# Kernel tuning notes

Measured on AMD Instinct MI355X. Metric: run time of the kernel, lower is better.

Reference implementation:

```python
import jax, jax.numpy as jnp
import numpy as np

IMG = 640.0
CONF_THRE = 0.05
NMS_THRE = 0.5
MAX_DET = 100          # fixed NMS output slots (padded with zeros / valid-masked)
PRE_NMS_TOPK = 1000    # candidates kept before NMS
NEG = -1e9
CLS_OFFSET = 4096.0    # batched_nms class-offset trick (> max coordinate)


def _make_anchors():
    # YOLO-style grid anchors: 3 scales per location, strides 8/16/32 -> N = 25200
    levels = []
    for s in (8, 16, 32):
        g = int(IMG) // s
        c = (np.arange(g, dtype=np.float32) + 0.5) * s
        cy, cx = np.meshgrid(c, c, indexing="ij")
        cx, cy = cx.reshape(-1), cy.reshape(-1)
        for scale in (0.5, 1.0, 2.0):
            w = s * 4.0 * scale
            levels.append(np.stack([cx - w / 2, cy - w / 2, cx + w / 2, cy + w / 2], 1))
    return np.concatenate(levels, 0).astype(np.float32)  # [25200, 4]


def setup_inputs() -> dict:
    key = jax.random.key(0)
    k1, k2 = jax.random.split(key)
    B, N, C = 16, 25200, 80
    return {
        "proposals_regs": jax.random.uniform(k1, (B, N, 5), dtype=jnp.float32),
        "proposals_clses": jax.random.uniform(k2, (B, N, C), dtype=jnp.float32),
        "anchors": jnp.asarray(_make_anchors()),
    }


def _decode(deltas, anchors):
    # standard delta decode relative to anchors, then clip to image (clip_bboxes)
    aw = anchors[:, 2] - anchors[:, 0]
    ah = anchors[:, 3] - anchors[:, 1]
    acx = (anchors[:, 0] + anchors[:, 2]) * 0.5
    acy = (anchors[:, 1] + anchors[:, 3]) * 0.5
    cx = acx + deltas[:, 0] * aw
    cy = acy + deltas[:, 1] * ah
    w = aw * jnp.exp(deltas[:, 2])
    h = ah * jnp.exp(deltas[:, 3])
    boxes = jnp.stack([cx - w / 2, cy - h / 2, cx + w / 2, cy + h / 2], 1)
    return jnp.clip(boxes, 0.0, IMG)


def _iou_one(box, boxes):
    lt = jnp.maximum(box[:2], boxes[:, :2])
    rb = jnp.minimum(box[2:], boxes[:, 2:])
    wh = jnp.clip(rb - lt, 0.0)
    inter = wh[:, 0] * wh[:, 1]
    a = (box[2] - box[0]) * (box[3] - box[1])
    b = (boxes[:, 2] - boxes[:, 0]) * (boxes[:, 3] - boxes[:, 1])
    union = a + b - inter
    return jnp.where(union > 0, inter / union, 0.0)


def _nms(boxes, scores):
    # greedy hard NMS with fixed MAX_DET iterations (jit-safe, fixed shapes)
    def body(i, st):
        sc, keep, ks = st
        best = jnp.argmax(sc)
        keep = keep.at[i].set(best.astype(jnp.int32))
        ks = ks.at[i].set(sc[best])
        sc = jnp.where(_iou_one(boxes[best], boxes) > NMS_THRE, NEG, sc)
        sc = sc.at[best].set(NEG)
        return sc, keep, ks
    keep0 = jnp.zeros((MAX_DET,), jnp.int32)
    ks0 = jnp.full((MAX_DET,), NEG, scores.dtype)
    _, keep, ks = jax.lax.fori_loop(0, MAX_DET, body, (scores, keep0, ks0))
    return keep, ks


def _per_image(reg, cls, anchors):
    p_obj = reg[:, 4]
    boxes = _decode(reg[:, :4], anchors)                     # [N,4] clipped xyxy
    class_conf = jnp.max(cls, axis=1)
    class_pred = jax.lax.stop_gradient(jnp.argmax(cls, axis=1))
    scores = p_obj * class_conf                              # batched_nms score
    scores = jnp.where(scores >= CONF_THRE, scores, NEG)     # confidence mask
    top_s, top_i = jax.lax.top_k(scores, PRE_NMS_TOPK)
    b = boxes[top_i]
    cp = class_pred[top_i].astype(boxes.dtype)
    obj = p_obj[top_i]
    cc = class_conf[top_i]
    off_boxes = b + cp[:, None] * CLS_OFFSET                 # per-class NMS
    keep, kept_scores = _nms(off_boxes, top_s)
    valid = kept_scores > NEG * 0.5
    det = jnp.concatenate(
        [b[keep], obj[keep][:, None], cc[keep][:, None], cp[keep][:, None]], 1
    )  # [MAX_DET, 7] = x1,y1,x2,y2,obj,conf,cls (same layout as torch code)
    return jnp.where(valid[:, None], det, 0.0)


def reference(proposals_regs, proposals_clses, anchors):
    return jax.vmap(lambda r, c: _per_image(r, c, anchors))(
        proposals_regs, proposals_clses
    )  # [B, MAX_DET, 7]
```

## Files before the change

### kernel.cpp

```cpp
#include <hip/hip_runtime.h>
#include <math.h>

#define BB 16
#define NN 25200
#define NCLS 80
#define TOPK 1000
#define MAXDET 100
#define CAND_CAP 2048
#define RANKS 1024
#define HBINS 1024
#define HBASE 0xBD00u
#define BPI_C 99
static constexpr float NEGV = -1000000000.0f;
static constexpr float IMGSZ = 640.0f;

struct Meta {
  unsigned b1;
  unsigned n_true;
  unsigned cnt;
  unsigned pad;
};

__device__ __forceinline__ unsigned flipKey(float f) {
  unsigned u = __float_as_uint(f);
  return (u & 0x80000000u) ? ~u : (u | 0x80000000u);
}
__device__ __forceinline__ float unflipKey(unsigned k) {
  unsigned u = (k & 0x80000000u) ? (k & 0x7FFFFFFFu) : ~k;
  return __uint_as_float(u);
}

#define UMAX_DPP(VAR, CTRL)                                                                   \
  {                                                                                           \
    unsigned _o = (unsigned)__builtin_amdgcn_update_dpp(0, (int)(VAR), CTRL, 0xF, 0xF, true); \
    if (_o > (VAR)) (VAR) = _o;                                                               \
  }

__global__ void __launch_bounds__(256) k_zero(unsigned* __restrict__ p) {
  p[blockIdx.x * 256 + threadIdx.x] = 0u;
}

__global__ void __launch_bounds__(256) k_score(const float* __restrict__ regs,
                                               const float* __restrict__ clses,
                                               unsigned* __restrict__ keys,
                                               float* __restrict__ ccs,
                                               int* __restrict__ preds,
                                               unsigned* __restrict__ hist1) {
  int t = blockIdx.x * 256 + threadIdx.x;
  int row = t >> 1, e = t & 1;
  const float4* r4 = reinterpret_cast<const float4*>(clses + (size_t)row * NCLS);
  float best = -1.0f;
  int bi = 0;
#pragma unroll
  for (int j = 0; j < 10; ++j) {
    int f = e + 2 * j;
    float4 v = r4[f];
    int b0 = f * 4;
    if (v.x > best) { best = v.x; bi = b0 + 0; }
    if (v.y > best) { best = v.y; bi = b0 + 1; }
    if (v.z > best) { best = v.z; bi = b0 + 2; }
    if (v.w > best) { best = v.w; bi = b0 + 3; }
  }
  unsigned vb = __float_as_uint(best);
  unsigned m = vb;
  UMAX_DPP(m, 0xB1);
  unsigned t2 = (vb == m) ? (unsigned)(79 - bi) : 0u;
  UMAX_DPP(t2, 0xB1);
  if (e == 0) {
    float bestv = __uint_as_float(m);
    int bidx = 79 - (int)t2;
    float pobj = regs[(size_t)row * 5 + 4];
    float sc = pobj * bestv;
    bool pass = (sc >= 0.05f);
    float s = pass ? sc : NEGV;
    unsigned key = flipKey(s);
    keys[row] = key;
    ccs[row] = bestv;
    preds[row] = bidx;
    if (pass) {
      unsigned bin = (key >> 16) - HBASE;
      atomicAdd(&hist1[(size_t)(row / NN) * HBINS + bin], 1u);
    }
  }
}

__global__ void __launch_bounds__(256) k_scan(const unsigned* __restrict__ hist,
                                              Meta* __restrict__ meta) {
  __shared__ unsigned part[256];
  __shared__ unsigned sfx[256];
  __shared__ int s_sel;
  __shared__ unsigned s_cum;
  int img = blockIdx.x;
  int t = threadIdx.x;
  const unsigned* h = hist + (size_t)img * HBINS;
  uint4 mine = reinterpret_cast<const uint4*>(h)[t];
  unsigned s = mine.x + mine.y + mine.z + mine.w;
  if (t == 0) { s_sel = -1; s_cum = 0; }
  part[t] = s;
  sfx[t] = s;
  __syncthreads();
  for (int d = 1; d < 256; d <<= 1) {
    unsigned v = (t + d < 256) ? sfx[t + d] : 0u;
    __syncthreads();
    sfx[t] += v;
    __syncthreads();
  }
  {
    unsigned incl = sfx[t];
    unsigned excl = incl - part[t];
    if (incl >= (unsigned)TOPK && excl < (unsigned)TOPK) { s_sel = t; s_cum = excl; }
  }
  __syncthreads();
  unsigned total = sfx[0];
  if (total < (unsigned)TOPK) {
    if (t == 0) {
      meta[img].b1 = HBASE + 1;
      meta[img].n_true = total;
    }
  } else if (t == s_sel) {
    unsigned cum = s_cum;
    unsigned vals[4] = {mine.x, mine.y, mine.z, mine.w};
    int sel = 0;
    unsigned c_ge = 0;
    for (int j = 3; j >= 0; --j) {
      if (cum + vals[j] >= (unsigned)TOPK) { sel = j; c_ge = cum + vals[j]; break; }
      cum += vals[j];
    }
    meta[img].b1 = HBASE + (unsigned)(4 * t + sel);
    meta[img].n_true = (c_ge > (unsigned)TOPK) ? (unsigned)TOPK : c_ge;
  }
}

__global__ void k_compact(const float* __restrict__ regs, const float* __restrict__ anchors,
                          const unsigned* __restrict__ keys, const float* __restrict__ ccs,
                          const int* __restrict__ preds, Meta* __restrict__ meta,
                          float* __restrict__ cand) {
  const size_t S2 = (size_t)BB * CAND_CAP;
  int img = blockIdx.x / BPI_C;
  int i = (blockIdx.x % BPI_C) * 256 + threadIdx.x;
  if (i >= NN) return;
  int lane = threadIdx.x & 63;
  unsigned long long lt = (1ull << lane) - 1ull;
  size_t g = (size_t)img * NN + (size_t)i;
  unsigned key = keys[g];
  bool take = (key >> 16) >= meta[img].b1;
  unsigned long long mA = __ballot(take);
  if (!take) return;
  int leader = __builtin_ctzll(mA);
  unsigned base = 0;
  if (lane == leader) base = atomicAdd(&meta[img].cnt, (unsigned)__popcll(mA));
  base = __shfl(base, leader);
  unsigned pos = base + (unsigned)__popcll(mA & lt);
  if (pos >= CAND_CAP) return;
  const float* r = regs + g * 5;
  float d0 = r[0], d1 = r[1], d2 = r[2], d3 = r[3], obj = r[4];
  const float* a = anchors + (size_t)i * 4;
  float ax1 = a[0], ay1 = a[1], ax2 = a[2], ay2 = a[3];
  float aw = ax2 - ax1, ah = ay2 - ay1;
  float acx = (ax1 + ax2) * 0.5f, acy = (ay1 + ay2) * 0.5f;
  float cx = acx + d0 * aw, cy = acy + d1 * ah;
  float w = aw * expf(d2), h = ah * expf(d3);
  float hw = 0.5f * w, hh = 0.5f * h;
  float x1 = fminf(fmaxf(cx - hw, 0.0f), IMGSZ);
  float y1 = fminf(fmaxf(cy - hh, 0.0f), IMGSZ);
  float x2 = fminf(fmaxf(cx + hw, 0.0f), IMGSZ);
  float y2 = fminf(fmaxf(cy + hh, 0.0f), IMGSZ);
  size_t o = (size_t)img * CAND_CAP + pos;
  cand[0 * S2 + o] = x1;
  cand[1 * S2 + o] = y1;
  cand[2 * S2 + o] = x2;
  cand[3 * S2 + o] = y2;
  cand[4 * S2 + o] = obj;
  cand[5 * S2 + o] = ccs[g];
  cand[6 * S2 + o] = (float)preds[g];
  cand[7 * S2 + o] = unflipKey(key);
  reinterpret_cast<unsigned*>(cand + 8 * S2)[o] = (unsigned)i;
}

__global__ void __launch_bounds__(256) k_rank(const float* __restrict__ cand,
                                              const Meta* __restrict__ meta,
                                              float* __restrict__ boxr,
                                              float4* __restrict__ payr0,
                                              float4* __restrict__ payr1) {
  const size_t S2 = (size_t)BB * CAND_CAP;
  const int NR = BB * RANKS;
  __shared__ unsigned long long kk[CAND_CAP];
  int img = blockIdx.x >> 5;
  int part = blockIdx.x & 31;
  int tid = threadIdx.x;
  unsigned nload = meta[img].cnt;
  if (nload > CAND_CAP) nload = CAND_CAP;
  for (int i = tid; i < CAND_CAP; i += 256) {
    unsigned long long kv = 0ull;
    if (i < (int)nload) {
      float sc = cand[7 * S2 + (size_t)img * CAND_CAP + i];
      unsigned ai = reinterpret_cast<const unsigned*>(cand + 8 * S2)[(size_t)img * CAND_CAP + i];
      kv = ((unsigned long long)flipKey(sc) << 16) |
           (unsigned long long)((0x7FFFu - ai) & 0xFFFFu);
    }
    kk[i] = kv;
  }
  __syncthreads();
  int slot = part * 64 + (tid >> 2);
  int qtr = tid & 3;
  unsigned long long myk = kk[slot];
  unsigned rank = 0;
  for (int q = qtr * 512; q < qtr * 512 + 512; ++q) rank += (kk[q] > myk) ? 1u : 0u;
  rank += (unsigned)__builtin_amdgcn_update_dpp(0, (int)rank, 0xB1, 0xF, 0xF, true);
  rank += (unsigned)__builtin_amdgcn_update_dpp(0, (int)rank, 0x4E, 0xF, 0xF, true);
  if (qtr == 0 && slot < (int)nload && rank < RANKS) {
    size_t o = (size_t)img * CAND_CAP + slot;
    float x1 = cand[0 * S2 + o], y1 = cand[1 * S2 + o];
    float x2 = cand[2 * S2 + o], y2 = cand[3 * S2 + o];
    float obj = cand[4 * S2 + o], cc = cand[5 * S2 + o];
    float cp = cand[6 * S2 + o], sc = cand[7 * S2 + o];
    float offv = cp * 4096.0f;
    float a1 = x1 + offv, b1v = y1 + offv, a2 = x2 + offv, b2v = y2 + offv;
    size_t ro = (size_t)img * RANKS + rank;
    boxr[0 * NR + ro] = a1;
    boxr[1 * NR + ro] = b1v;
    boxr[2 * NR + ro] = a2;
    boxr[3 * NR + ro] = b2v;
    boxr[4 * NR + ro] = (a2 - a1) * (b2v - b1v);
    payr0[ro] = make_float4(x1, y1, x2, y2);
    payr1[ro] = make_float4(obj, cc, cp, sc);
  }
}

__global__ void __launch_bounds__(256) k_matrix(const float* __restrict__ boxr,
                                                const Meta* __restrict__ meta,
                                                unsigned long long* __restrict__ mat) {
  const int NR = BB * RANKS;
  __shared__ float sx1[RANKS], sy1[RANKS], sx2[RANKS], sy2[RANKS], sar[RANKS];
  int img = blockIdx.x >> 6;
  int part = blockIdx.x & 63;
  int tid = threadIdx.x, lane = tid & 63, wid = tid >> 6;
  for (int i = tid; i < RANKS; i += 256) {
    int g = img * RANKS + i;
    sx1[i] = boxr[0 * NR + g];
    sy1[i] = boxr[1 * NR + g];
    sx2[i] = boxr[2 * NR + g];
    sy2[i] = boxr[3 * NR + g];
    sar[i] = boxr[4 * NR + g];
  }
  unsigned n = meta[img].n_true;
  __syncthreads();
#pragma unroll
  for (int rr = 0; rr < 4; ++rr) {
    int r = part * 16 + wid * 4 + rr;
    if (r >= (int)n) continue;
    float bx1 = sx1[r], by1 = sy1[r], bx2 = sx2[r], by2 = sy2[r], bA = sar[r];
    unsigned long long* rowp = mat + ((size_t)img * RANKS + r) * 16;
#pragma unroll
    for (int w2 = 0; w2 < 16; ++w2) {
      int c = w2 * 64 + lane;
      float lx = fmaxf(bx1, sx1[c]), ly = fmaxf(by1, sy1[c]);
      float rx = fminf(bx2, sx2[c]), ry = fminf(by2, sy2[c]);
      float iw = fmaxf(rx - lx, 0.f), ih = fmaxf(ry - ly, 0.f);
      float inter = iw * ih;
      float uu = bA + sar[c] - inter;
      float ss = fmaf(2.0f, inter, -uu);
      float tt = uu * 0x1p-24f;
      bool sup = (uu > 0.f && ss > tt) || (c == r);
      unsigned long long b = __ballot(sup);
      if (lane == w2) rowp[w2] = b;
    }
  }
}

__global__ void __launch_bounds__(256, 1) k_scan2(const unsigned long long* __restrict__ mat,
                                                  const Meta* __restrict__ meta,
                                                  const float4* __restrict__ payr0,
                                                  const float4* __restrict__ payr1,
                                                  float* __restrict__ out) {
  __shared__ unsigned long long smat[RANKS * 16];
  __shared__ unsigned wins[MAXDET];
  __shared__ float4 lout4[MAXDET * 7 / 4];
  int img = blockIdx.x, tid = threadIdx.x, lane = tid & 63, wid = tid >> 6;
  const uint4* gm = reinterpret_cast<const uint4*>(mat + (size_t)img * RANKS * 16);
  uint4* sm4 = reinterpret_cast<uint4*>(smat);
  for (int i = tid; i < RANKS * 16 / 2; i += 256) sm4[i] = gm[i];
  if (tid < MAXDET) wins[tid] = 0xFFFFFFFFu;
  unsigned n = meta[img].n_true;
  __syncthreads();
  if (wid == 0) {
    unsigned long long alive = 0ull;
    if (lane < 16) {
      int lo = lane * 64;
      alive = ((int)n >= lo + 64) ? ~0ull
                                  : (((int)n > lo) ? ((1ull << ((int)n - lo)) - 1ull) : 0ull);
    }
    for (int it = 0; it < MAXDET; ++it) {
      unsigned long long any = __ballot(alive != 0ull);
      if (any == 0ull) break;
      int f = __builtin_ctzll(any);
      unsigned long long w = __shfl(alive, f);
      int r = f * 64 + __builtin_ctzll(w);
      if (lane == 0) wins[it] = (unsigned)r;
      unsigned long long rowv = (lane < 16) ? smat[r * 16 + lane] : 0ull;
      alive &= ~rowv;
    }
  }
  __syncthreads();
  if (tid < MAXDET) {
    unsigned r = wins[tid];
    float* row = reinterpret_cast<float*>(lout4) + tid * 7;
    if (r == 0xFFFFFFFFu) {
      row[0] = 0.f; row[1] = 0.f; row[2] = 0.f; row[3] = 0.f;
      row[4] = 0.f; row[5] = 0.f; row[6] = 0.f;
    } else {
      float4 p0 = payr0[(size_t)img * RANKS + r];
      float4 p1 = payr1[(size_t)img * RANKS + r];
      row[0] = p0.x; row[1] = p0.y; row[2] = p0.z; row[3] = p0.w;
      row[4] = p1.x; row[5] = p1.y; row[6] = p1.z;
    }
  }
  __syncthreads();
  float4* go4 = reinterpret_cast<float4*>(out + (size_t)img * MAXDET * 7);
  if (tid < MAXDET * 7 / 4) go4[tid] = lout4[tid];
}

extern "C" void kernel_launch(void* const* d_in, const int* in_sizes, int n_in,
                              void* d_out, int out_size, void* d_ws, size_t ws_size,
                              hipStream_t stream) {
  const float* regs = (const float*)d_in[0];
  const float* clses = (const float*)d_in[1];
  const float* anchors = (const float*)d_in[2];
  float* out = (float*)d_out;
  char* ws = (char*)d_ws;

  constexpr size_t HIST_BYTES = (size_t)BB * HBINS * 4;
  constexpr size_t META_OFF = HIST_BYTES;
  constexpr size_t META_BYTES = 1024;
  constexpr size_t KEYS_OFF = META_OFF + META_BYTES;
  constexpr size_t ARR_BYTES = (size_t)BB * NN * 4;
  constexpr size_t CCS_OFF = KEYS_OFF + ARR_BYTES;
  constexpr size_t PREDS_OFF = CCS_OFF + ARR_BYTES;
  constexpr size_t CAND_OFF = PREDS_OFF + ARR_BYTES;
  constexpr size_t CAND_BYTES = (size_t)9 * BB * CAND_CAP * 4;
  constexpr size_t BOXR_OFF = CAND_OFF + CAND_BYTES;
  constexpr size_t BOXR_BYTES = (size_t)5 * BB * RANKS * 4;
  constexpr size_t PAYR_OFF = BOXR_OFF + BOXR_BYTES;
  constexpr size_t PAYR_BYTES = (size_t)2 * BB * RANKS * 16;
  constexpr size_t MAT_OFF = PAYR_OFF + PAYR_BYTES;

  unsigned* hist1 = (unsigned*)(ws);
  Meta* meta = (Meta*)(ws + META_OFF);
  unsigned* keys = (unsigned*)(ws + KEYS_OFF);
  float* ccs = (float*)(ws + CCS_OFF);
  int* preds = (int*)(ws + PREDS_OFF);
  float* cand = (float*)(ws + CAND_OFF);
  float* boxr = (float*)(ws + BOXR_OFF);
  float4* payr0 = (float4*)(ws + PAYR_OFF);
  float4* payr1 = (float4*)(ws + PAYR_OFF + (size_t)BB * RANKS * 16);
  unsigned long long* mat = (unsigned long long*)(ws + MAT_OFF);

  k_zero<<<(int)(KEYS_OFF / 1024), 256, 0, stream>>>((unsigned*)ws);

  k_score<<<BB * NN * 2 / 256, 256, 0, stream>>>(regs, clses, keys, ccs, preds, hist1);
  k_scan<<<BB, 256, 0, stream>>>(hist1, meta);
  k_compact<<<BB * BPI_C, 256, 0, stream>>>(regs, anchors, keys, ccs, preds, meta, cand);
  k_rank<<<BB * 32, 256, 0, stream>>>(cand, meta, boxr, payr0, payr1);
  k_matrix<<<BB * 64, 256, 0, stream>>>(boxr, meta, mat);
  k_scan2<<<BB, 256, 0, stream>>>(mat, meta, payr0, payr1, out);
}
```

Before: 170.0 us.

## Prefilter rows by objectness histogram before reading class scores

Replaces the single scoring pass with a staged selection. First a histogram of objectness finds a cutoff, and class maxima are computed only for rows above it. A second score histogram then gives a lower bound, and a further pass covers only rows whose objectness lies between that bound and the first cutoff. This relies on score = pobj*max_cls ≤ pobj, which needs class scores in [0,1], and is meant to avoid streaming the full 80-class tensor. It adds two extra scan launches and a pkey array, and rows never visited keep zeroed keys, with stale ccs/preds entries.

After: 154.6 us (median of 2 runs). -9.1%, faster.

```diff
diff --git a/kernel.cpp b/kernel.cpp
--- a/kernel.cpp
+++ b/kernel.cpp
@@ -15,10 +15,12 @@
 static constexpr float IMGSZ = 640.0f;
 
 struct Meta {
+  unsigned b1p;
+  unsigned b1c;
   unsigned b1;
   unsigned n_true;
   unsigned cnt;
-  unsigned pad;
+  unsigned pad0, pad1, pad2;
 };
 
 __device__ __forceinline__ unsigned flipKey(float f) {
@@ -30,62 +32,23 @@
   return __uint_as_float(u);
 }
 
-#define UMAX_DPP(VAR, CTRL)                                                                   \
-  {                                                                                           \
-    unsigned _o = (unsigned)__builtin_amdgcn_update_dpp(0, (int)(VAR), CTRL, 0xF, 0xF, true); \
-    if (_o > (VAR)) (VAR) = _o;                                                               \
-  }
-
 __global__ void __launch_bounds__(256) k_zero(unsigned* __restrict__ p) {
   p[blockIdx.x * 256 + threadIdx.x] = 0u;
 }
 
-__global__ void __launch_bounds__(256) k_score(const float* __restrict__ regs,
-                                               const float* __restrict__ clses,
-                                               unsigned* __restrict__ keys,
-                                               float* __restrict__ ccs,
-                                               int* __restrict__ preds,
-                                               unsigned* __restrict__ hist1) {
-  int t = blockIdx.x * 256 + threadIdx.x;
-  int row = t >> 1, e = t & 1;
-  const float4* r4 = reinterpret_cast<const float4*>(clses + (size_t)row * NCLS);
-  float best = -1.0f;
-  int bi = 0;
-#pragma unroll
-  for (int j = 0; j < 10; ++j) {
-    int f = e + 2 * j;
-    float4 v = r4[f];
-    int b0 = f * 4;
-    if (v.x > best) { best = v.x; bi = b0 + 0; }
-    if (v.y > best) { best = v.y; bi = b0 + 1; }
-    if (v.z > best) { best = v.z; bi = b0 + 2; }
-    if (v.w > best) { best = v.w; bi = b0 + 3; }
-  }
-  unsigned vb = __float_as_uint(best);
-  unsigned m = vb;
-  UMAX_DPP(m, 0xB1);
-  unsigned t2 = (vb == m) ? (unsigned)(79 - bi) : 0u;
-  UMAX_DPP(t2, 0xB1);
-  if (e == 0) {
-    float bestv = __uint_as_float(m);
-    int bidx = 79 - (int)t2;
-    float pobj = regs[(size_t)row * 5 + 4];
-    float sc = pobj * bestv;
-    bool pass = (sc >= 0.05f);
-    float s = pass ? sc : NEGV;
-    unsigned key = flipKey(s);
-    keys[row] = key;
-    ccs[row] = bestv;
-    preds[row] = bidx;
-    if (pass) {
-      unsigned bin = (key >> 16) - HBASE;
-      atomicAdd(&hist1[(size_t)(row / NN) * HBINS + bin], 1u);
-    }
-  }
+__global__ void __launch_bounds__(256) k_pobj(const float* __restrict__ regs,
+                                              unsigned* __restrict__ pkey,
+                                              unsigned* __restrict__ histp) {
+  int g = blockIdx.x * 256 + threadIdx.x;
+  float pobj = regs[(size_t)g * 5 + 4];
+  unsigned key = flipKey(pobj);
+  pkey[g] = key;
+  if (pobj >= 0.05f)
+    atomicAdd(&histp[(size_t)(g / NN) * HBINS + ((key >> 16) - HBASE)], 1u);
 }
 
 __global__ void __launch_bounds__(256) k_scan(const unsigned* __restrict__ hist,
-                                              Meta* __restrict__ meta) {
+                                              Meta* __restrict__ meta, int mode) {
   __shared__ unsigned part[256];
   __shared__ unsigned sfx[256];
   __shared__ int s_sel;
@@ -114,8 +77,9 @@
   unsigned total = sfx[0];
   if (total < (unsigned)TOPK) {
     if (t == 0) {
-      meta[img].b1 = HBASE + 1;
-      meta[img].n_true = total;
+      if (mode == 0) meta[img].b1p = HBASE + 1;
+      else if (mode == 1) meta[img].b1c = HBASE + 1;
+      else { meta[img].b1 = HBASE + 1; meta[img].n_true = total; }
     }
   } else if (t == s_sel) {
     unsigned cum = s_cum;
@@ -126,9 +90,51 @@
       if (cum + vals[j] >= (unsigned)TOPK) { sel = j; c_ge = cum + vals[j]; break; }
       cum += vals[j];
     }
-    meta[img].b1 = HBASE + (unsigned)(4 * t + sel);
-    meta[img].n_true = (c_ge > (unsigned)TOPK) ? (unsigned)TOPK : c_ge;
-  }
+    unsigned bin = HBASE + (unsigned)(4 * t + sel);
+    if (mode == 0) meta[img].b1p = bin;
+    else if (mode == 1) meta[img].b1c = bin;
+    else {
+      meta[img].b1 = bin;
+      meta[img].n_true = (c_ge > (unsigned)TOPK) ? (unsigned)TOPK : c_ge;
+    }
+  }
+}
+
+__global__ void __launch_bounds__(256) k_cand(const float* __restrict__ regs,
+                                              const float* __restrict__ clses,
+                                              const unsigned* __restrict__ pkey,
+                                              const Meta* __restrict__ meta,
+                                              unsigned* __restrict__ keys,
+                                              float* __restrict__ ccs,
+                                              int* __restrict__ preds,
+                                              unsigned* __restrict__ hists, int mode) {
+  int g = blockIdx.x * 256 + threadIdx.x;
+  int img = g / NN;
+  unsigned pk = pkey[g];
+  unsigned pk16 = pk >> 16;
+  unsigned lo = (mode == 0) ? meta[img].b1p : meta[img].b1c;
+  unsigned hi = (mode == 0) ? 0x10000u : meta[img].b1p;
+  if (pk16 < lo || pk16 >= hi) return;
+  const float4* r4 = reinterpret_cast<const float4*>(clses + (size_t)g * NCLS);
+  float best = -1.0f;
+  int bi = 0;
+#pragma unroll
+  for (int f = 0; f < 20; ++f) {
+    float4 v = r4[f];
+    int b0 = f * 4;
+    if (v.x > best) { best = v.x; bi = b0 + 0; }
+    if (v.y > best) { best = v.y; bi = b0 + 1; }
+    if (v.z > best) { best = v.z; bi = b0 + 2; }
+    if (v.w > best) { best = v.w; bi = b0 + 3; }
+  }
+  float pobj = unflipKey(pk);
+  float sc = pobj * best;
+  bool pass = (sc >= 0.05f);
+  unsigned key = flipKey(pass ? sc : NEGV);
+  keys[g] = key;
+  ccs[g] = best;
+  preds[g] = bi;
+  if (pass) atomicAdd(&hists[(size_t)img * HBINS + ((key >> 16) - HBASE)], 1u);
 }
 
 __global__ void k_compact(const float* __restrict__ regs, const float* __restrict__ anchors,
@@ -329,14 +335,16 @@
   float* out = (float*)d_out;
   char* ws = (char*)d_ws;
 
-  constexpr size_t HIST_BYTES = (size_t)BB * HBINS * 4;
-  constexpr size_t META_OFF = HIST_BYTES;
-  constexpr size_t META_BYTES = 1024;
-  constexpr size_t KEYS_OFF = META_OFF + META_BYTES;
+  constexpr size_t HISTP_OFF = 0;
+  constexpr size_t HISTS_OFF = 65536;
+  constexpr size_t META_OFF = 131072;
+  constexpr size_t KEYS_OFF = 132096;
   constexpr size_t ARR_BYTES = (size_t)BB * NN * 4;
+  constexpr size_t ZERO_BYTES = KEYS_OFF + ARR_BYTES;
   constexpr size_t CCS_OFF = KEYS_OFF + ARR_BYTES;
   constexpr size_t PREDS_OFF = CCS_OFF + ARR_BYTES;
-  constexpr size_t CAND_OFF = PREDS_OFF + ARR_BYTES;
+  constexpr size_t PKEY_OFF = PREDS_OFF + ARR_BYTES;
+  constexpr size_t CAND_OFF = PKEY_OFF + ARR_BYTES;
   constexpr size_t CAND_BYTES = (size_t)9 * BB * CAND_CAP * 4;
   constexpr size_t BOXR_OFF = CAND_OFF + CAND_BYTES;
   constexpr size_t BOXR_BYTES = (size_t)5 * BB * RANKS * 4;
@@ -344,21 +352,28 @@
   constexpr size_t PAYR_BYTES = (size_t)2 * BB * RANKS * 16;
   constexpr size_t MAT_OFF = PAYR_OFF + PAYR_BYTES;
 
-  unsigned* hist1 = (unsigned*)(ws);
+  unsigned* histp = (unsigned*)(ws + HISTP_OFF);
+  unsigned* hists = (unsigned*)(ws + HISTS_OFF);
   Meta* meta = (Meta*)(ws + META_OFF);
   unsigned* keys = (unsigned*)(ws + KEYS_OFF);
   float* ccs = (float*)(ws + CCS_OFF);
   int* preds = (int*)(ws + PREDS_OFF);
+  unsigned* pkey = (unsigned*)(ws + PKEY_OFF);
   float* cand = (float*)(ws + CAND_OFF);
   float* boxr = (float*)(ws + BOXR_OFF);
   float4* payr0 = (float4*)(ws + PAYR_OFF);
   float4* payr1 = (float4*)(ws + PAYR_OFF + (size_t)BB * RANKS * 16);
   unsigned long long* mat = (unsigned long long*)(ws + MAT_OFF);
 
-  k_zero<<<(int)(KEYS_OFF / 1024), 256, 0, stream>>>((unsigned*)ws);
-
-  k_score<<<BB * NN * 2 / 256, 256, 0, stream>>>(regs, clses, keys, ccs, preds, hist1);
-  k_scan<<<BB, 256, 0, stream>>>(hist1, meta);
+  k_zero<<<(int)(ZERO_BYTES / 1024), 256, 0, stream>>>((unsigned*)ws);
+
+  int rblocks = BB * NN / 256;
+  k_pobj<<<rblocks, 256, 0, stream>>>(regs, pkey, histp);
+  k_scan<<<BB, 256, 0, stream>>>(histp, meta, 0);
+  k_cand<<<rblocks, 256, 0, stream>>>(regs, clses, pkey, meta, keys, ccs, preds, hists, 0);
+  k_scan<<<BB, 256, 0, stream>>>(hists, meta, 1);
+  k_cand<<<rblocks, 256, 0, stream>>>(regs, clses, pkey, meta, keys, ccs, preds, hists, 1);
+  k_scan<<<BB, 256, 0, stream>>>(hists, meta, 2);
   k_compact<<<BB * BPI_C, 256, 0, stream>>>(regs, anchors, keys, ccs, preds, meta, cand);
   k_rank<<<BB * 32, 256, 0, stream>>>(cand, meta, boxr, payr0, payr1);
   k_matrix<<<BB * 64, 256, 0, stream>>>(boxr, meta, mat);
```
